# Performance work log

Measured on AMD Instinct MI355X. Metric: run time of the kernel, lower is better.

The kernel has to match this reference:

```python
import jax, jax.numpy as jnp
import numpy as np

B = 262144
T = 50000
F = 19
E = 16
H = 128
D = 64
S = 3
EPS = 1e-5


def setup_inputs() -> dict:
    key = jax.random.key(0)
    ks = jax.random.split(key, 20)
    inp = {
        'home_team': jax.random.randint(ks[0], (B,), 0, T),
        'away_team': jax.random.randint(ks[1], (B,), 0, T),
        'game_features': jax.random.normal(ks[2], (B, F), dtype=jnp.float32),
        'sport_id': jax.random.randint(ks[3], (B,), 0, S),
        # parameters
        'emb_home': jax.random.normal(ks[4], (T, E), dtype=jnp.float32) * 0.1,
        'emb_away': jax.random.normal(ks[5], (T, E), dtype=jnp.float32) * 0.1,
        'W_gf': jax.random.normal(ks[6], (F, E), dtype=jnp.float32) * 0.2,
        'b_gf': jnp.zeros((E,), dtype=jnp.float32),
        'W_sh': jax.random.normal(ks[7], (3 * E, H), dtype=jnp.float32) * 0.1,
        'b_sh': jnp.zeros((H,), dtype=jnp.float32),
        'bn_gamma': jnp.ones((H,), dtype=jnp.float32),
        'bn_beta': jnp.zeros((H,), dtype=jnp.float32),
        'bn_mean': jax.random.normal(ks[8], (H,), dtype=jnp.float32) * 0.05,
        'bn_var': jax.random.uniform(ks[9], (H,), dtype=jnp.float32, minval=0.5, maxval=1.5),
        'W_exp': jax.random.normal(ks[10], (S, H, D), dtype=jnp.float32) * 0.1,
        'b_exp': jnp.zeros((S, D), dtype=jnp.float32),
        'ln_gamma': jnp.ones((S, D), dtype=jnp.float32),
        'ln_beta': jnp.zeros((S, D), dtype=jnp.float32),
        'W_out': jax.random.normal(ks[11], (D, 1), dtype=jnp.float32) * 0.1,
        'b_out': jnp.zeros((1,), dtype=jnp.float32),
    }
    return inp


def _forward(home_team, away_team, game_features, sport_id,
             emb_home, emb_away, W_gf, b_gf, W_sh, b_sh,
             bn_gamma, bn_beta, bn_mean, bn_var,
             W_exp, b_exp, ln_gamma, ln_beta, W_out, b_out):
    he = emb_home[home_team]                                  # [B, E]
    ae = emb_away[away_team]                                  # [B, E]
    gf = jax.nn.relu(game_features @ W_gf + b_gf)             # [B, E]
    x = jnp.concatenate([he, ae, gf], axis=-1)                # [B, 3E]
    # shared_fc: Linear + BatchNorm1d (eval: running stats) + ReLU (+ Dropout noop)
    s = x @ W_sh + b_sh                                       # [B, H]
    s = (s - bn_mean) * jax.lax.rsqrt(bn_var + EPS) * bn_gamma + bn_beta
    s = jax.nn.relu(s)
    # masked expert dispatch: static loop over S=3 experts, select by sport_id
    out = jnp.zeros((s.shape[0], D), dtype=s.dtype)
    for i in range(S):
        h = s @ W_exp[i] + b_exp[i]                           # [B, D]
        m = jnp.mean(h, axis=-1, keepdims=True)
        v = jnp.mean((h - m) ** 2, axis=-1, keepdims=True)
        hn = (h - m) * jax.lax.rsqrt(v + EPS) * ln_gamma[i] + ln_beta[i]
        h = jax.nn.relu(hn)
        out = jnp.where((sport_id == i)[:, None], h, out)
    return jax.nn.sigmoid(out @ W_out + b_out)                # [B, 1]


def reference(home_team, away_team, game_features, sport_id,
              emb_home, emb_away, W_gf, b_gf, W_sh, b_sh,
              bn_gamma, bn_beta, bn_mean, bn_var,
              W_exp, b_exp, ln_gamma, ln_beta, W_out, b_out):
    return _forward(home_team, away_team, game_features, sport_id,
                    emb_home, emb_away, W_gf, b_gf, W_sh, b_sh,
                    bn_gamma, bn_beta, bn_mean, bn_var,
                    W_exp, b_exp, ln_gamma, ln_beta, W_out, b_out)
```

## Files before the change

### kernel.cpp

```cpp
#include <hip/hip_runtime.h>
#include <hip/hip_bf16.h>
#include <stdint.h>

#define DEV_INLINE __device__ __forceinline__

typedef short          short8 __attribute__((ext_vector_type(8)));
typedef unsigned short u16x8  __attribute__((ext_vector_type(8)));
typedef unsigned int   u32x4  __attribute__((ext_vector_type(4)));
typedef float          f32x4  __attribute__((ext_vector_type(4)));

constexpr int   MB_  = 128;
constexpr int   BLKT = 256;
constexpr float EPSV = 1e-5f;

#define XIDX(r,c)  (((r)<<6) + ((((c)>>3) ^ ((r)&7))<<3)  + ((c)&7))
#define WSIDX(c,k) (((c)<<6) + ((((k)>>3) ^ ((c)&7))<<3)  + ((k)&7))
#define SIDX(r,j)  (((r)<<7) + ((((j)>>3) ^ ((r)&15))<<3) + ((j)&7))
#define WEIDX(c,k) (((c)<<7) + ((((k)>>3) ^ ((c)&15))<<3) + ((k)&7))

static DEV_INLINE unsigned short f2bf(float f) {
    return __builtin_bit_cast(unsigned short, __float2bfloat16(f));
}

__global__ __launch_bounds__(BLKT, 2) void fused_kernel(
    const int*   __restrict__ home,  const int* __restrict__ away,
    const float* __restrict__ gfeat, const int* __restrict__ sport,
    const float* __restrict__ emb_h, const float* __restrict__ emb_a,
    const float* __restrict__ W_gf,  const float* __restrict__ b_gf,
    const float* __restrict__ W_sh,  const float* __restrict__ b_sh,
    const float* __restrict__ bn_g,  const float* __restrict__ bn_b,
    const float* __restrict__ bn_m,  const float* __restrict__ bn_v,
    const float* __restrict__ Wexp,  const float* __restrict__ bexp,
    const float* __restrict__ ln_g,  const float* __restrict__ ln_b,
    const float* __restrict__ wout,  const float* __restrict__ bo,
    float* __restrict__ out)
{
    __shared__ __align__(16) unsigned char smem[65536];
    unsigned short* Xl = (unsigned short*)(smem);
    unsigned short* Wl = (unsigned short*)(smem + 16384);
    unsigned short* Sl = (unsigned short*)(smem + 32768);

    const int tid  = threadIdx.x;
    const int r0   = blockIdx.x * MB_;
    const int lane = tid & 63;
    const int w    = tid >> 6;
    const int llo  = lane & 15;
    const int lhi  = lane >> 4;

    if (tid < 128) {
        const int r = r0 + tid;
        float x[48];
        {
            const int ht = home[r], at = away[r];
            const float4* ph = (const float4*)(emb_h + (size_t)ht * 16);
            const float4* pa = (const float4*)(emb_a + (size_t)at * 16);
#pragma unroll
            for (int q = 0; q < 4; ++q) { float4 v = ph[q]; x[q*4]=v.x; x[q*4+1]=v.y; x[q*4+2]=v.z; x[q*4+3]=v.w; }
#pragma unroll
            for (int q = 0; q < 4; ++q) { float4 v = pa[q]; x[16+q*4]=v.x; x[16+q*4+1]=v.y; x[16+q*4+2]=v.z; x[16+q*4+3]=v.w; }
            float gl[19];
            const float* gr = gfeat + (size_t)r * 19;
#pragma unroll
            for (int f = 0; f < 19; ++f) gl[f] = gr[f];
            float ag[16];
#pragma unroll
            for (int e = 0; e < 16; ++e) ag[e] = b_gf[e];
#pragma unroll 2
            for (int f = 0; f < 19; ++f) {
                const float* wf = W_gf + f * 16;
#pragma unroll
                for (int e = 0; e < 16; ++e) ag[e] = fmaf(gl[f], wf[e], ag[e]);
            }
#pragma unroll
            for (int e = 0; e < 16; ++e) x[32+e] = fmaxf(ag[e], 0.f);
        }
#pragma unroll
        for (int g = 0; g < 8; ++g) {
            u16x8 v;
#pragma unroll
            for (int j = 0; j < 8; ++j) {
                const int c = g*8 + j;
                v[j] = (c < 48) ? f2bf(x[c]) : (unsigned short)0;
            }
            *(u32x4*)&Xl[XIDX(tid, g*8)] = __builtin_bit_cast(u32x4, v);
        }
    } else {
        const int c2 = tid - 128;
        float wk[48];
#pragma unroll 8
        for (int k = 0; k < 48; ++k) wk[k] = W_sh[k * 128 + c2];
#pragma unroll
        for (int g = 0; g < 8; ++g) {
            u16x8 v;
#pragma unroll
            for (int j = 0; j < 8; ++j) {
                const int k = g*8 + j;
                v[j] = (k < 48) ? f2bf(wk[k]) : (unsigned short)0;
            }
            *(u32x4*)&Wl[WSIDX(c2, g*8)] = __builtin_bit_cast(u32x4, v);
        }
    }
    __syncthreads();

    f32x4 acc[2][8];
#pragma unroll
    for (int mt = 0; mt < 2; ++mt)
#pragma unroll
        for (int nt = 0; nt < 8; ++nt) acc[mt][nt] = (f32x4){0.f, 0.f, 0.f, 0.f};

#pragma unroll
    for (int kk = 0; kk < 2; ++kk) {
        short8 a0 = *(const short8*)&Xl[XIDX((w*2+0)*16 + llo, kk*32 + lhi*8)];
        short8 a1 = *(const short8*)&Xl[XIDX((w*2+1)*16 + llo, kk*32 + lhi*8)];
#pragma unroll
        for (int nt = 0; nt < 8; ++nt) {
            short8 b = *(const short8*)&Wl[WSIDX(nt*16 + llo, kk*32 + lhi*8)];
            acc[0][nt] = __builtin_amdgcn_mfma_f32_16x16x32_bf16(a0, b, acc[0][nt], 0, 0, 0);
            acc[1][nt] = __builtin_amdgcn_mfma_f32_16x16x32_bf16(a1, b, acc[1][nt], 0, 0, 0);
        }
    }

    const int cs  = tid & 63;
    const int kg0 = (tid >> 6) * 4;
    float stg[4][8];
#pragma unroll
    for (int i = 0; i < 4; ++i)
#pragma unroll
        for (int j = 0; j < 8; ++j)
            stg[i][j] = Wexp[((kg0 + i)*8 + j) * 64 + cs];

#pragma unroll
    for (int nt = 0; nt < 8; ++nt) {
        const int col = nt*16 + llo;
        const float sc = bn_g[col] * rsqrtf(bn_v[col] + EPSV);
        const float sh = (b_sh[col] - bn_m[col]) * sc + bn_b[col];
#pragma unroll
        for (int e = 0; e < 4; ++e) {
            const int ro = (w*2)*16 + lhi*4 + e;
            Sl[SIDX(ro,      col)] = f2bf(fmaxf(fmaf(acc[0][nt][e], sc, sh), 0.f));
            Sl[SIDX(ro + 16, col)] = f2bf(fmaxf(fmaf(acc[1][nt][e], sc, sh), 0.f));
        }
    }
    __syncthreads();

    {
        unsigned short* B0 = (unsigned short*)smem;
#pragma unroll
        for (int i = 0; i < 4; ++i) {
            u16x8 v;
#pragma unroll
            for (int j = 0; j < 8; ++j) v[j] = f2bf(stg[i][j]);
            *(u32x4*)&B0[WEIDX(cs, (kg0 + i)*8)] = __builtin_bit_cast(u32x4, v);
        }
    }
    __syncthreads();

    short8 af[2][4];
#pragma unroll
    for (int mt = 0; mt < 2; ++mt)
#pragma unroll
        for (int kk = 0; kk < 4; ++kk)
            af[mt][kk] = *(const short8*)&Sl[SIDX((w*2+mt)*16 + llo, kk*32 + lhi*8)];

    int spv[2][4];
#pragma unroll
    for (int mt = 0; mt < 2; ++mt)
#pragma unroll
        for (int e = 0; e < 4; ++e)
            spv[mt][e] = sport[r0 + (w*2+mt)*16 + lhi*4 + e];

    f32x4 acce[2][12];
#pragma unroll
    for (int mt = 0; mt < 2; ++mt)
#pragma unroll
        for (int t = 0; t < 12; ++t) acce[mt][t] = (f32x4){0.f, 0.f, 0.f, 0.f};

#pragma unroll
    for (int s = 0; s < 3; ++s) {
        if (s < 2) {
#pragma unroll
            for (int i = 0; i < 4; ++i)
#pragma unroll
                for (int j = 0; j < 8; ++j)
                    stg[i][j] = Wexp[(s+1)*8192 + ((kg0 + i)*8 + j)*64 + cs];
        }
        const unsigned short* Bc = (const unsigned short*)smem + (s & 1) * 8192;
#pragma unroll
        for (int kk = 0; kk < 4; ++kk) {
#pragma unroll
            for (int nt = 0; nt < 4; ++nt) {
                short8 b = *(const short8*)&Bc[WEIDX(nt*16 + llo, kk*32 + lhi*8)];
                acce[0][s*4+nt] = __builtin_amdgcn_mfma_f32_16x16x32_bf16(af[0][kk], b, acce[0][s*4+nt], 0, 0, 0);
                acce[1][s*4+nt] = __builtin_amdgcn_mfma_f32_16x16x32_bf16(af[1][kk], b, acce[1][s*4+nt], 0, 0, 0);
            }
        }
        if (s < 2) {
            unsigned short* Bn = (unsigned short*)smem + ((s+1) & 1) * 8192;
#pragma unroll
            for (int i = 0; i < 4; ++i) {
                u16x8 v;
#pragma unroll
                for (int j = 0; j < 8; ++j) v[j] = f2bf(stg[i][j]);
                *(u32x4*)&Bn[WEIDX(cs, (kg0 + i)*8)] = __builtin_bit_cast(u32x4, v);
            }
            __syncthreads();
        }
    }

    float wo[4], lgp[3][4], lbp[3][4], bep[3][4];
#pragma unroll
    for (int nt = 0; nt < 4; ++nt) wo[nt] = wout[nt*16 + llo];
#pragma unroll
    for (int s = 0; s < 3; ++s)
#pragma unroll
        for (int nt = 0; nt < 4; ++nt) {
            lgp[s][nt] = ln_g[s*64 + nt*16 + llo];
            lbp[s][nt] = ln_b[s*64 + nt*16 + llo];
            bep[s][nt] = bexp[s*64 + nt*16 + llo];
        }
    const float bo0 = bo[0];

#pragma unroll
    for (int mt = 0; mt < 2; ++mt) {
#pragma unroll
        for (int e = 0; e < 4; ++e) {
            const int rl = (w*2+mt)*16 + lhi*4 + e;
            const int sp = spv[mt][e];
            float h[4];
#pragma unroll
            for (int nt = 0; nt < 4; ++nt) {
                float v  = (sp == 0) ? acce[mt][nt][e] : (sp == 1 ? acce[mt][4+nt][e] : acce[mt][8+nt][e]);
                float bb = (sp == 0) ? bep[0][nt]      : (sp == 1 ? bep[1][nt]        : bep[2][nt]);
                h[nt] = v + bb;
            }
            float m = (h[0] + h[1]) + (h[2] + h[3]);
            m += __shfl_xor(m, 1); m += __shfl_xor(m, 2); m += __shfl_xor(m, 4); m += __shfl_xor(m, 8);
            m *= (1.0f / 64.0f);
            float vv = 0.f;
#pragma unroll
            for (int nt = 0; nt < 4; ++nt) { float c = h[nt] - m; vv = fmaf(c, c, vv); }
            vv += __shfl_xor(vv, 1); vv += __shfl_xor(vv, 2); vv += __shfl_xor(vv, 4); vv += __shfl_xor(vv, 8);
            const float inv = rsqrtf(vv * (1.0f / 64.0f) + EPSV);
            float z = 0.f;
#pragma unroll
            for (int nt = 0; nt < 4; ++nt) {
                float g_ = (sp == 0) ? lgp[0][nt] : (sp == 1 ? lgp[1][nt] : lgp[2][nt]);
                float b_ = (sp == 0) ? lbp[0][nt] : (sp == 1 ? lbp[1][nt] : lbp[2][nt]);
                float hn = fmaf((h[nt] - m) * inv, g_, b_);
                hn = fmaxf(hn, 0.f);
                z  = fmaf(hn, wo[nt], z);
            }
            z += __shfl_xor(z, 1); z += __shfl_xor(z, 2); z += __shfl_xor(z, 4); z += __shfl_xor(z, 8);
            if (llo == 0) out[r0 + rl] = 1.0f / (1.0f + __expf(-(z + bo0)));
        }
    }
}

extern "C" void kernel_launch(void* const* d_in, const int* in_sizes, int n_in,
                              void* d_out, int out_size, void* d_ws, size_t ws_size,
                              hipStream_t stream) {
    const int*   home  = (const int*)  d_in[0];
    const int*   away  = (const int*)  d_in[1];
    const float* gf    = (const float*)d_in[2];
    const int*   sport = (const int*)  d_in[3];
    const float* emb_h = (const float*)d_in[4];
    const float* emb_a = (const float*)d_in[5];
    const float* W_gf  = (const float*)d_in[6];
    const float* b_gf  = (const float*)d_in[7];
    const float* W_sh  = (const float*)d_in[8];
    const float* b_sh  = (const float*)d_in[9];
    const float* bn_g  = (const float*)d_in[10];
    const float* bn_b  = (const float*)d_in[11];
    const float* bn_m  = (const float*)d_in[12];
    const float* bn_v  = (const float*)d_in[13];
    const float* Wexp  = (const float*)d_in[14];
    const float* bexp  = (const float*)d_in[15];
    const float* ln_g  = (const float*)d_in[16];
    const float* ln_b  = (const float*)d_in[17];
    const float* wout  = (const float*)d_in[18];
    const float* bo    = (const float*)d_in[19];
    float* out = (float*)d_out;

    const int B = in_sizes[0];
    fused_kernel<<<B / MB_, BLKT, 0, stream>>>(home, away, gf, sport, emb_h, emb_a,
                                               W_gf, b_gf, W_sh, b_sh,
                                               bn_g, bn_b, bn_m, bn_v,
                                               Wexp, bexp, ln_g, ln_b, wout, bo, out);
}
```

Baseline: 174.6 us.

## Pre-pack weights into MFMA fragment layout and make main kernel wave-independent

Adds a prep kernel that converts W_sh and W_exp to bf16 already laid out in MFMA B-fragment order, and folds the batchnorm scale and shift into per-column constants stored in workspace. The main kernel then loads B fragments straight from global/L2 with no shared-memory staging and no block-level barriers. Each wave builds its own A fragments from the embedding gathers and a lane-split game-feature matmul reduced with a shuffle. Expert outputs are selected per row as each expert finishes, which cuts accumulator register pressure. The cost is an extra launch and repeated global weight reads in every wave.

Measured after the change: 179.1 us. +2.6%, slower.

```diff
diff --git a/kernel.cpp b/kernel.cpp
--- a/kernel.cpp
+++ b/kernel.cpp
@@ -5,253 +5,233 @@
 #define DEV_INLINE __device__ __forceinline__
 
 typedef short          short8 __attribute__((ext_vector_type(8)));
+typedef unsigned short u16;
 typedef unsigned short u16x8  __attribute__((ext_vector_type(8)));
-typedef unsigned int   u32x4  __attribute__((ext_vector_type(4)));
 typedef float          f32x4  __attribute__((ext_vector_type(4)));
 
-constexpr int   MB_  = 128;
-constexpr int   BLKT = 256;
 constexpr float EPSV = 1e-5f;
 
-#define XIDX(r,c)  (((r)<<6) + ((((c)>>3) ^ ((r)&7))<<3)  + ((c)&7))
-#define WSIDX(c,k) (((c)<<6) + ((((k)>>3) ^ ((c)&7))<<3)  + ((k)&7))
+
+static DEV_INLINE u16 f2bf(float f) {
+    return __builtin_bit_cast(u16, __float2bfloat16(f));
+}
+
+__global__ void prep_kernel(const float* __restrict__ W_gf,
+                            const float* __restrict__ W_sh, const float* __restrict__ b_sh,
+                            const float* __restrict__ bn_g, const float* __restrict__ bn_b,
+                            const float* __restrict__ bn_m, const float* __restrict__ bn_v,
+                            const float* __restrict__ Wexp,
+                            unsigned char* __restrict__ ws)
+{
+    const int gid = blockIdx.x * blockDim.x + threadIdx.x;
+    u16*   wshF = (u16*)ws;
+    u16*   wexF = (u16*)(ws + 16384);
+    float* scp  = (float*)(ws + 65536);
+    float* shp  = (float*)(ws + 66048);
+    float* wgp  = (float*)(ws + 66560);
+
+    if (gid < 8192) {
+        const int fid = gid >> 9, l = (gid >> 3) & 63, j = gid & 7;
+        const int kk = fid >> 3, nt = fid & 7;
+        const int k = kk*32 + ((l >> 4) << 3) + j;
+        const int c = nt*16 + (l & 15);
+        wshF[gid] = f2bf((k < 48) ? W_sh[k*128 + c] : 0.f);
+    } else {
+        const int id = gid - 8192;
+        const int fid = id >> 9, l = (id >> 3) & 63, j = id & 7;
+        const int s = fid >> 4, kk = (fid >> 2) & 3, nt = fid & 3;
+        const int k = kk*32 + ((l >> 4) << 3) + j;
+        const int d = nt*16 + (l & 15);
+        wexF[id] = f2bf(Wexp[s*8192 + k*64 + d]);
+    }
+    if (gid < 128) {
+        const float sc = bn_g[gid] * rsqrtf(bn_v[gid] + EPSV);
+        scp[gid] = sc;
+        shp[gid] = (b_sh[gid] - bn_m[gid]) * sc + bn_b[gid];
+    }
+    if (gid < 320) {
+        const int f = gid >> 4, e = gid & 15;
+        wgp[gid] = (f < 19) ? W_gf[f*16 + e] : 0.f;
+    }
+}
+
 #define SIDX(r,j)  (((r)<<7) + ((((j)>>3) ^ ((r)&15))<<3) + ((j)&7))
-#define WEIDX(c,k) (((c)<<7) + ((((k)>>3) ^ ((c)&15))<<3) + ((k)&7))
-
-static DEV_INLINE unsigned short f2bf(float f) {
-    return __builtin_bit_cast(unsigned short, __float2bfloat16(f));
-}
-
-__global__ __launch_bounds__(BLKT, 2) void fused_kernel(
+
+__global__ __launch_bounds__(256) void fused_kernel(
     const int*   __restrict__ home,  const int* __restrict__ away,
     const float* __restrict__ gfeat, const int* __restrict__ sport,
     const float* __restrict__ emb_h, const float* __restrict__ emb_a,
-    const float* __restrict__ W_gf,  const float* __restrict__ b_gf,
-    const float* __restrict__ W_sh,  const float* __restrict__ b_sh,
-    const float* __restrict__ bn_g,  const float* __restrict__ bn_b,
-    const float* __restrict__ bn_m,  const float* __restrict__ bn_v,
-    const float* __restrict__ Wexp,  const float* __restrict__ bexp,
+    const float* __restrict__ b_gf,
+    const float* __restrict__ bexp,
     const float* __restrict__ ln_g,  const float* __restrict__ ln_b,
     const float* __restrict__ wout,  const float* __restrict__ bo,
+    const unsigned char* __restrict__ ws,
     float* __restrict__ out)
 {
-    __shared__ __align__(16) unsigned char smem[65536];
-    unsigned short* Xl = (unsigned short*)(smem);
-    unsigned short* Wl = (unsigned short*)(smem + 16384);
-    unsigned short* Sl = (unsigned short*)(smem + 32768);
+    __shared__ __align__(16) u16 Sl[4][32 * 128];
 
     const int tid  = threadIdx.x;
-    const int r0   = blockIdx.x * MB_;
     const int lane = tid & 63;
     const int w    = tid >> 6;
     const int llo  = lane & 15;
     const int lhi  = lane >> 4;
-
-    if (tid < 128) {
-        const int r = r0 + tid;
-        float x[48];
-        {
-            const int ht = home[r], at = away[r];
-            const float4* ph = (const float4*)(emb_h + (size_t)ht * 16);
-            const float4* pa = (const float4*)(emb_a + (size_t)at * 16);
-#pragma unroll
-            for (int q = 0; q < 4; ++q) { float4 v = ph[q]; x[q*4]=v.x; x[q*4+1]=v.y; x[q*4+2]=v.z; x[q*4+3]=v.w; }
-#pragma unroll
-            for (int q = 0; q < 4; ++q) { float4 v = pa[q]; x[16+q*4]=v.x; x[16+q*4+1]=v.y; x[16+q*4+2]=v.z; x[16+q*4+3]=v.w; }
-            float gl[19];
-            const float* gr = gfeat + (size_t)r * 19;
-#pragma unroll
-            for (int f = 0; f < 19; ++f) gl[f] = gr[f];
-            float ag[16];
-#pragma unroll
-            for (int e = 0; e < 16; ++e) ag[e] = b_gf[e];
-#pragma unroll 2
-            for (int f = 0; f < 19; ++f) {
-                const float* wf = W_gf + f * 16;
-#pragma unroll
-                for (int e = 0; e < 16; ++e) ag[e] = fmaf(gl[f], wf[e], ag[e]);
+    const int r0w  = blockIdx.x * 128 + w * 32;
+
+    const u16*   wshF = (const u16*)ws;
+    const u16*   wexF = (const u16*)(ws + 16384);
+    const float* scp  = (const float*)(ws + 65536);
+    const float* shp  = (const float*)(ws + 66048);
+    const float* wgp  = (const float*)(ws + 66560);
+
+    short8 a[2][2];
+    {
+        const int*   idxp = (lhi < 2) ? home  : away;
+        const float* tab  = (lhi < 2) ? emb_h : emb_a;
+        const int    off  = (lhi & 1) * 8;
+#pragma unroll
+        for (int mt = 0; mt < 2; ++mt) {
+            const int r = r0w + mt*16 + llo;
+            const float* rp = tab + (size_t)idxp[r] * 16 + off;
+            const float4 v0 = *(const float4*)rp;
+            const float4 v1 = *(const float4*)(rp + 4);
+            u16x8 p;
+            p[0]=f2bf(v0.x); p[1]=f2bf(v0.y); p[2]=f2bf(v0.z); p[3]=f2bf(v0.w);
+            p[4]=f2bf(v1.x); p[5]=f2bf(v1.y); p[6]=f2bf(v1.z); p[7]=f2bf(v1.w);
+            a[mt][0] = __builtin_bit_cast(short8, p);
+        }
+    }
+    {
+        const int eo = (lhi & 1) * 8;
+        const int f0 = (lhi >> 1) * 10;
+        float p0[8] = {0,0,0,0,0,0,0,0}, p1[8] = {0,0,0,0,0,0,0,0};
+#pragma unroll
+        for (int i = 0; i < 10; ++i) {
+            const int f  = f0 + i;
+            const int fc = (f < 19) ? f : 18;
+            const float4 w0 = *(const float4*)(wgp + f*16 + eo);
+            const float4 w1 = *(const float4*)(wgp + f*16 + eo + 4);
+            const float g0 = gfeat[(size_t)(r0w + llo)      * 19 + fc];
+            const float g1 = gfeat[(size_t)(r0w + 16 + llo) * 19 + fc];
+            p0[0]=fmaf(g0,w0.x,p0[0]); p0[1]=fmaf(g0,w0.y,p0[1]); p0[2]=fmaf(g0,w0.z,p0[2]); p0[3]=fmaf(g0,w0.w,p0[3]);
+            p0[4]=fmaf(g0,w1.x,p0[4]); p0[5]=fmaf(g0,w1.y,p0[5]); p0[6]=fmaf(g0,w1.z,p0[6]); p0[7]=fmaf(g0,w1.w,p0[7]);
+            p1[0]=fmaf(g1,w0.x,p1[0]); p1[1]=fmaf(g1,w0.y,p1[1]); p1[2]=fmaf(g1,w0.z,p1[2]); p1[3]=fmaf(g1,w0.w,p1[3]);
+            p1[4]=fmaf(g1,w1.x,p1[4]); p1[5]=fmaf(g1,w1.y,p1[5]); p1[6]=fmaf(g1,w1.z,p1[6]); p1[7]=fmaf(g1,w1.w,p1[7]);
+        }
+        const float4 bg0 = *(const float4*)(b_gf + eo);
+        const float4 bg1 = *(const float4*)(b_gf + eo + 4);
+        const float bg[8] = {bg0.x,bg0.y,bg0.z,bg0.w,bg1.x,bg1.y,bg1.z,bg1.w};
+        u16x8 q0, q1;
+#pragma unroll
+        for (int j = 0; j < 8; ++j) {
+            const float s0 = p0[j] + __shfl_xor(p0[j], 32);
+            const float s1 = p1[j] + __shfl_xor(p1[j], 32);
+            q0[j] = (lhi < 2) ? f2bf(fmaxf(s0 + bg[j], 0.f)) : (u16)0;
+            q1[j] = (lhi < 2) ? f2bf(fmaxf(s1 + bg[j], 0.f)) : (u16)0;
+        }
+        a[0][1] = __builtin_bit_cast(short8, q0);
+        a[1][1] = __builtin_bit_cast(short8, q1);
+    }
+
+    u16* sl = &Sl[w][0];
+#pragma unroll
+    for (int nt = 0; nt < 8; ++nt) {
+        const short8 b0 = *(const short8*)(wshF + (0*8 + nt)*512 + lane*8);
+        const short8 b1 = *(const short8*)(wshF + (1*8 + nt)*512 + lane*8);
+        f32x4 c0 = {0.f,0.f,0.f,0.f}, c1 = {0.f,0.f,0.f,0.f};
+        c0 = __builtin_amdgcn_mfma_f32_16x16x32_bf16(a[0][0], b0, c0, 0, 0, 0);
+        c0 = __builtin_amdgcn_mfma_f32_16x16x32_bf16(a[0][1], b1, c0, 0, 0, 0);
+        c1 = __builtin_amdgcn_mfma_f32_16x16x32_bf16(a[1][0], b0, c1, 0, 0, 0);
+        c1 = __builtin_amdgcn_mfma_f32_16x16x32_bf16(a[1][1], b1, c1, 0, 0, 0);
+        const int col = nt*16 + llo;
+        const float sc = scp[col], sh = shp[col];
+#pragma unroll
+        for (int e = 0; e < 4; ++e) {
+            sl[SIDX(lhi*4 + e,      col)] = f2bf(fmaxf(fmaf(c0[e], sc, sh), 0.f));
+            sl[SIDX(16 + lhi*4 + e, col)] = f2bf(fmaxf(fmaf(c1[e], sc, sh), 0.f));
+        }
+    }
+
+    short8 af[2][4];
+#pragma unroll
+    for (int mt = 0; mt < 2; ++mt)
+#pragma unroll
+        for (int kk = 0; kk < 4; ++kk)
+            af[mt][kk] = *(const short8*)&sl[SIDX(mt*16 + llo, kk*32 + lhi*8)];
+
+    int spv[2][4];
+#pragma unroll
+    for (int mt = 0; mt < 2; ++mt)
+#pragma unroll
+        for (int e = 0; e < 4; ++e)
+            spv[mt][e] = sport[r0w + mt*16 + lhi*4 + e];
+
+    float h[2][4][4];
+#pragma unroll
+    for (int s = 0; s < 3; ++s) {
+        f32x4 ac[2][4];
+#pragma unroll
+        for (int mt = 0; mt < 2; ++mt)
+#pragma unroll
+            for (int nt = 0; nt < 4; ++nt) ac[mt][nt] = (f32x4){0.f,0.f,0.f,0.f};
+#pragma unroll
+        for (int nt = 0; nt < 4; ++nt) {
+#pragma unroll
+            for (int kk = 0; kk < 4; ++kk) {
+                const short8 b = *(const short8*)(wexF + ((s*4 + kk)*4 + nt)*512 + lane*8);
+                ac[0][nt] = __builtin_amdgcn_mfma_f32_16x16x32_bf16(af[0][kk], b, ac[0][nt], 0, 0, 0);
+                ac[1][nt] = __builtin_amdgcn_mfma_f32_16x16x32_bf16(af[1][kk], b, ac[1][nt], 0, 0, 0);
             }
-#pragma unroll
-            for (int e = 0; e < 16; ++e) x[32+e] = fmaxf(ag[e], 0.f);
-        }
-#pragma unroll
-        for (int g = 0; g < 8; ++g) {
-            u16x8 v;
-#pragma unroll
-            for (int j = 0; j < 8; ++j) {
-                const int c = g*8 + j;
-                v[j] = (c < 48) ? f2bf(x[c]) : (unsigned short)0;
-            }
-            *(u32x4*)&Xl[XIDX(tid, g*8)] = __builtin_bit_cast(u32x4, v);
-        }
-    } else {
-        const int c2 = tid - 128;
-        float wk[48];
-#pragma unroll 8
-        for (int k = 0; k < 48; ++k) wk[k] = W_sh[k * 128 + c2];
-#pragma unroll
-        for (int g = 0; g < 8; ++g) {
-            u16x8 v;
-#pragma unroll
-            for (int j = 0; j < 8; ++j) {
-                const int k = g*8 + j;
-                v[j] = (k < 48) ? f2bf(wk[k]) : (unsigned short)0;
-            }
-            *(u32x4*)&Wl[WSIDX(c2, g*8)] = __builtin_bit_cast(u32x4, v);
-        }
-    }
-    __syncthreads();
-
-    f32x4 acc[2][8];
-#pragma unroll
-    for (int mt = 0; mt < 2; ++mt)
-#pragma unroll
-        for (int nt = 0; nt < 8; ++nt) acc[mt][nt] = (f32x4){0.f, 0.f, 0.f, 0.f};
-
-#pragma unroll
-    for (int kk = 0; kk < 2; ++kk) {
-        short8 a0 = *(const short8*)&Xl[XIDX((w*2+0)*16 + llo, kk*32 + lhi*8)];
-        short8 a1 = *(const short8*)&Xl[XIDX((w*2+1)*16 + llo, kk*32 + lhi*8)];
-#pragma unroll
-        for (int nt = 0; nt < 8; ++nt) {
-            short8 b = *(const short8*)&Wl[WSIDX(nt*16 + llo, kk*32 + lhi*8)];
-            acc[0][nt] = __builtin_amdgcn_mfma_f32_16x16x32_bf16(a0, b, acc[0][nt], 0, 0, 0);
-            acc[1][nt] = __builtin_amdgcn_mfma_f32_16x16x32_bf16(a1, b, acc[1][nt], 0, 0, 0);
-        }
-    }
-
-    const int cs  = tid & 63;
-    const int kg0 = (tid >> 6) * 4;
-    float stg[4][8];
-#pragma unroll
-    for (int i = 0; i < 4; ++i)
-#pragma unroll
-        for (int j = 0; j < 8; ++j)
-            stg[i][j] = Wexp[((kg0 + i)*8 + j) * 64 + cs];
-
-#pragma unroll
-    for (int nt = 0; nt < 8; ++nt) {
+        }
+#pragma unroll
+        for (int nt = 0; nt < 4; ++nt) {
+            const float bb = bexp[s*64 + nt*16 + llo];
+#pragma unroll
+            for (int mt = 0; mt < 2; ++mt)
+#pragma unroll
+                for (int e = 0; e < 4; ++e) {
+                    const float cand = ac[mt][nt][e] + bb;
+                    const bool take = (spv[mt][e] == s);
+                    h[mt][nt][e] = (s == 0) ? (take ? cand : 0.f)
+                                            : (take ? cand : h[mt][nt][e]);
+                }
+        }
+    }
+
+    float wo[4], lg0[4], lg1[4], lg2[4], lb0[4], lb1[4], lb2[4];
+#pragma unroll
+    for (int nt = 0; nt < 4; ++nt) {
         const int col = nt*16 + llo;
-        const float sc = bn_g[col] * rsqrtf(bn_v[col] + EPSV);
-        const float sh = (b_sh[col] - bn_m[col]) * sc + bn_b[col];
+        wo[nt]  = wout[col];
+        lg0[nt] = ln_g[col];       lb0[nt] = ln_b[col];
+        lg1[nt] = ln_g[64 + col];  lb1[nt] = ln_b[64 + col];
+        lg2[nt] = ln_g[128 + col]; lb2[nt] = ln_b[128 + col];
+    }
+    const float bo0 = bo[0];
+
+#pragma unroll
+    for (int mt = 0; mt < 2; ++mt) {
 #pragma unroll
         for (int e = 0; e < 4; ++e) {
-            const int ro = (w*2)*16 + lhi*4 + e;
-            Sl[SIDX(ro,      col)] = f2bf(fmaxf(fmaf(acc[0][nt][e], sc, sh), 0.f));
-            Sl[SIDX(ro + 16, col)] = f2bf(fmaxf(fmaf(acc[1][nt][e], sc, sh), 0.f));
-        }
-    }
-    __syncthreads();
-
-    {
-        unsigned short* B0 = (unsigned short*)smem;
-#pragma unroll
-        for (int i = 0; i < 4; ++i) {
-            u16x8 v;
-#pragma unroll
-            for (int j = 0; j < 8; ++j) v[j] = f2bf(stg[i][j]);
-            *(u32x4*)&B0[WEIDX(cs, (kg0 + i)*8)] = __builtin_bit_cast(u32x4, v);
-        }
-    }
-    __syncthreads();
-
-    short8 af[2][4];
-#pragma unroll
-    for (int mt = 0; mt < 2; ++mt)
-#pragma unroll
-        for (int kk = 0; kk < 4; ++kk)
-            af[mt][kk] = *(const short8*)&Sl[SIDX((w*2+mt)*16 + llo, kk*32 + lhi*8)];
-
-    int spv[2][4];
-#pragma unroll
-    for (int mt = 0; mt < 2; ++mt)
-#pragma unroll
-        for (int e = 0; e < 4; ++e)
-            spv[mt][e] = sport[r0 + (w*2+mt)*16 + lhi*4 + e];
-
-    f32x4 acce[2][12];
-#pragma unroll
-    for (int mt = 0; mt < 2; ++mt)
-#pragma unroll
-        for (int t = 0; t < 12; ++t) acce[mt][t] = (f32x4){0.f, 0.f, 0.f, 0.f};
-
-#pragma unroll
-    for (int s = 0; s < 3; ++s) {
-        if (s < 2) {
-#pragma unroll
-            for (int i = 0; i < 4; ++i)
-#pragma unroll
-                for (int j = 0; j < 8; ++j)
-                    stg[i][j] = Wexp[(s+1)*8192 + ((kg0 + i)*8 + j)*64 + cs];
-        }
-        const unsigned short* Bc = (const unsigned short*)smem + (s & 1) * 8192;
-#pragma unroll
-        for (int kk = 0; kk < 4; ++kk) {
-#pragma unroll
-            for (int nt = 0; nt < 4; ++nt) {
-                short8 b = *(const short8*)&Bc[WEIDX(nt*16 + llo, kk*32 + lhi*8)];
-                acce[0][s*4+nt] = __builtin_amdgcn_mfma_f32_16x16x32_bf16(af[0][kk], b, acce[0][s*4+nt], 0, 0, 0);
-                acce[1][s*4+nt] = __builtin_amdgcn_mfma_f32_16x16x32_bf16(af[1][kk], b, acce[1][s*4+nt], 0, 0, 0);
-            }
-        }
-        if (s < 2) {
-            unsigned short* Bn = (unsigned short*)smem + ((s+1) & 1) * 8192;
-#pragma unroll
-            for (int i = 0; i < 4; ++i) {
-                u16x8 v;
-#pragma unroll
-                for (int j = 0; j < 8; ++j) v[j] = f2bf(stg[i][j]);
-                *(u32x4*)&Bn[WEIDX(cs, (kg0 + i)*8)] = __builtin_bit_cast(u32x4, v);
-            }
-            __syncthreads();
-        }
-    }
-
-    float wo[4], lgp[3][4], lbp[3][4], bep[3][4];
-#pragma unroll
-    for (int nt = 0; nt < 4; ++nt) wo[nt] = wout[nt*16 + llo];
-#pragma unroll
-    for (int s = 0; s < 3; ++s)
-#pragma unroll
-        for (int nt = 0; nt < 4; ++nt) {
-            lgp[s][nt] = ln_g[s*64 + nt*16 + llo];
-            lbp[s][nt] = ln_b[s*64 + nt*16 + llo];
-            bep[s][nt] = bexp[s*64 + nt*16 + llo];
-        }
-    const float bo0 = bo[0];
-
-#pragma unroll
-    for (int mt = 0; mt < 2; ++mt) {
-#pragma unroll
-        for (int e = 0; e < 4; ++e) {
-            const int rl = (w*2+mt)*16 + lhi*4 + e;
             const int sp = spv[mt][e];
-            float h[4];
-#pragma unroll
-            for (int nt = 0; nt < 4; ++nt) {
-                float v  = (sp == 0) ? acce[mt][nt][e] : (sp == 1 ? acce[mt][4+nt][e] : acce[mt][8+nt][e]);
-                float bb = (sp == 0) ? bep[0][nt]      : (sp == 1 ? bep[1][nt]        : bep[2][nt]);
-                h[nt] = v + bb;
-            }
-            float m = (h[0] + h[1]) + (h[2] + h[3]);
+            float m = (h[mt][0][e] + h[mt][1][e]) + (h[mt][2][e] + h[mt][3][e]);
             m += __shfl_xor(m, 1); m += __shfl_xor(m, 2); m += __shfl_xor(m, 4); m += __shfl_xor(m, 8);
             m *= (1.0f / 64.0f);
             float vv = 0.f;
 #pragma unroll
-            for (int nt = 0; nt < 4; ++nt) { float c = h[nt] - m; vv = fmaf(c, c, vv); }
+            for (int nt = 0; nt < 4; ++nt) { const float c = h[mt][nt][e] - m; vv = fmaf(c, c, vv); }
             vv += __shfl_xor(vv, 1); vv += __shfl_xor(vv, 2); vv += __shfl_xor(vv, 4); vv += __shfl_xor(vv, 8);
             const float inv = rsqrtf(vv * (1.0f / 64.0f) + EPSV);
             float z = 0.f;
 #pragma unroll
             for (int nt = 0; nt < 4; ++nt) {
-                float g_ = (sp == 0) ? lgp[0][nt] : (sp == 1 ? lgp[1][nt] : lgp[2][nt]);
-                float b_ = (sp == 0) ? lbp[0][nt] : (sp == 1 ? lbp[1][nt] : lbp[2][nt]);
-                float hn = fmaf((h[nt] - m) * inv, g_, b_);
+                const float g_ = (sp == 0) ? lg0[nt] : (sp == 1 ? lg1[nt] : lg2[nt]);
+                const float b_ = (sp == 0) ? lb0[nt] : (sp == 1 ? lb1[nt] : lb2[nt]);
+                float hn = fmaf((h[mt][nt][e] - m) * inv, g_, b_);
                 hn = fmaxf(hn, 0.f);
                 z  = fmaf(hn, wo[nt], z);
             }
             z += __shfl_xor(z, 1); z += __shfl_xor(z, 2); z += __shfl_xor(z, 4); z += __shfl_xor(z, 8);
-            if (llo == 0) out[r0 + rl] = 1.0f / (1.0f + __expf(-(z + bo0)));
+            if (llo == 0) out[r0w + mt*16 + lhi*4 + e] = 1.0f / (1.0f + __expf(-(z + bo0)));
         }
     }
 }
@@ -280,10 +260,11 @@
     const float* wout  = (const float*)d_in[18];
     const float* bo    = (const float*)d_in[19];
     float* out = (float*)d_out;
+    unsigned char* ws = (unsigned char*)d_ws;
 
     const int B = in_sizes[0];
-    fused_kernel<<<B / MB_, BLKT, 0, stream>>>(home, away, gf, sport, emb_h, emb_a,
-                                               W_gf, b_gf, W_sh, b_sh,
-                                               bn_g, bn_b, bn_m, bn_v,
-                                               Wexp, bexp, ln_g, ln_b, wout, bo, out);
-}
+
+    prep_kernel<<<128, 256, 0, stream>>>(W_gf, W_sh, b_sh, bn_g, bn_b, bn_m, bn_v, Wexp, ws);
+    fused_kernel<<<B / 128, 256, 0, stream>>>(home, away, gf, sport, emb_h, emb_a,
+                                              b_gf, bexp, ln_g, ln_b, wout, bo, ws, out);
+}
```
